# Kernel tuning notes

Measured on AMD Instinct MI355X. Metric: run time of the kernel, lower is better.

The kernel has to match this reference:

```python
import jax, jax.numpy as jnp
import numpy as np

NUM_NODES = 50000
NUM_HYPEREDGES = 10000
NUM_INCIDENCES = 800000
CHANNELS = 256
NEG_SLOPE = 0.01  # torch leaky_relu default negative_slope


def setup_inputs() -> dict:
    key = jax.random.key(0)
    k_n, k_e, k_emb, k_cw, k_lw, k_lb = jax.random.split(key, 6)
    node_idx = jax.random.randint(k_n, (NUM_INCIDENCES,), 0, NUM_NODES, dtype=jnp.int32)
    edge_idx = jax.random.randint(k_e, (NUM_INCIDENCES,), 0, NUM_HYPEREDGES, dtype=jnp.int32)
    edge_index = jnp.stack([node_idx, edge_idx], axis=0)  # [2, nnz] incidence list
    s = 1.0 / np.sqrt(CHANNELS).astype(np.float32)
    emb = jax.random.normal(k_emb, (NUM_NODES, CHANNELS), jnp.float32)  # Node2Vec embedding table
    conv_w = jax.random.normal(k_cw, (CHANNELS, CHANNELS), jnp.float32) * s  # HypergraphConv.lin (no bias)
    conv_b = jnp.zeros((CHANNELS,), jnp.float32)  # HypergraphConv.bias
    lin_w = jax.random.normal(k_lw, (CHANNELS, CHANNELS), jnp.float32) * s
    lin_b = jax.random.normal(k_lb, (CHANNELS,), jnp.float32) * s
    return {"emb": emb, "conv_w": conv_w, "conv_b": conv_b,
            "lin_w": lin_w, "lin_b": lin_b, "edge_index": edge_index}


def reference(emb, conv_w, conv_b, lin_w, lin_b, edge_index):
    node_idx, edge_idx = edge_index[0], edge_index[1]
    # HypergraphConv (use_attention=False): X' = D^-1 H B^-1 H^T (X W^T) + b
    x = emb @ conv_w.T  # [N, C]
    ones = jnp.ones((NUM_INCIDENCES,), x.dtype)
    D = jax.ops.segment_sum(ones, node_idx, num_segments=NUM_NODES)       # node degree
    Dinv = jnp.where(D > 0, 1.0 / D, 0.0)
    B = jax.ops.segment_sum(ones, edge_idx, num_segments=NUM_HYPEREDGES)  # hyperedge degree
    Binv = jnp.where(B > 0, 1.0 / B, 0.0)
    # node -> hyperedge aggregation
    e = jax.ops.segment_sum(x[node_idx], edge_idx, num_segments=NUM_HYPEREDGES) * Binv[:, None]  # [E, C]
    # hyperedge -> node aggregation
    n = jax.ops.segment_sum(e[edge_idx], node_idx, num_segments=NUM_NODES) * Dinv[:, None] + conv_b  # [N, C]
    y = jax.nn.leaky_relu(n, NEG_SLOPE)
    g = y.T @ y  # [C, C] Gram
    out = jax.nn.leaky_relu(g @ lin_w.T + lin_b, NEG_SLOPE)
    return out
```

## Files before the change

### kernel.cpp

```cpp
#include <hip/hip_runtime.h>

#define N_NODES 50000
#define N_EDGES 10000
#define NNZ     800000
#define C       256
#define SLOPE   0.01f
#define KTOT    50176
#define KCHUNK  512
#define NZB     98
#define MPAD    10048

#define NB      250
#define EB_E    40
#define EB_N    200
#define CHUNK   3125
#define CAP     6000

#define EAGG_G  157
#define NAGG_G  784

#define OFF_CC_E    0
#define OFF_CC_N    1024
#define OFF_CUR_E   2048
#define OFF_CUR_N   3072
#define ZERO_BYTES  4096
#define OFF_CB_E    266240
#define OFF_CB_N    267264
#define OFF_RS_N    268288
#define OFF_RS_E    468480
#define OFF_BUF_E   508672
#define OFF_BUF_N   3708672
#define OFF_CSR_E   6908672
#define OFF_CSR_N   10108672
#define OFF_EMBH    13308672
#define OFF_YT      13308672
#define OFF_EACC    39000064
#define OFF_E2      44144640
#define OFF_CWH     49289216
#define OFF_PART    49420288

typedef __attribute__((ext_vector_type(8))) short short8;
typedef __attribute__((ext_vector_type(4))) float floatx4;

static __device__ __forceinline__ unsigned short f2bf(float f) {
    unsigned int u = __float_as_uint(f);
    u = (u + 0x7fffu + ((u >> 16) & 1u)) >> 16;
    return (unsigned short)u;
}

static __device__ __forceinline__ void acc_bf8(const uint4 d, float* a) {
    a[0] += __uint_as_float(d.x << 16);
    a[1] += __uint_as_float(d.x & 0xffff0000u);
    a[2] += __uint_as_float(d.y << 16);
    a[3] += __uint_as_float(d.y & 0xffff0000u);
    a[4] += __uint_as_float(d.z << 16);
    a[5] += __uint_as_float(d.z & 0xffff0000u);
    a[6] += __uint_as_float(d.w << 16);
    a[7] += __uint_as_float(d.w & 0xffff0000u);
}

__global__ __launch_bounds__(256) void zero_kernel(float4* __restrict__ p, int n4) {
    int i = blockIdx.x * 256 + threadIdx.x;
    if (i < n4) p[i] = make_float4(0.f, 0.f, 0.f, 0.f);
}

#define PREP_EMB_BLOCKS 6251
#define PREP_CW_BLOCKS  32
__global__ __launch_bounds__(256) void prep_kernel(const float4* __restrict__ emb4,
                                                   uint4* __restrict__ embh4,
                                                   const float4* __restrict__ cw4,
                                                   uint4* __restrict__ cwh4,
                                                   const int* __restrict__ node_idx,
                                                   const int* __restrict__ edge_idx,
                                                   int* __restrict__ cc_e,
                                                   int* __restrict__ cc_n) {
    __shared__ int he[NB], hn[NB];
    int b = blockIdx.x, tid = threadIdx.x;
    if (b < PREP_EMB_BLOCKS) {
        int i = b * 256 + tid;
        if (i >= 1600032) return;
        uint4 o = {0u, 0u, 0u, 0u};
        if (i < 1600000) {
            float4 f0 = emb4[2 * i], f1 = emb4[2 * i + 1];
            o.x = f2bf(f0.x) | ((unsigned)f2bf(f0.y) << 16);
            o.y = f2bf(f0.z) | ((unsigned)f2bf(f0.w) << 16);
            o.z = f2bf(f1.x) | ((unsigned)f2bf(f1.y) << 16);
            o.w = f2bf(f1.z) | ((unsigned)f2bf(f1.w) << 16);
        }
        int node = i >> 5, c = i & 31;
        embh4[(size_t)(((c >> 2) * 50001 + node) << 2) + (c & 3)] = o;
    } else if (b < PREP_EMB_BLOCKS + PREP_CW_BLOCKS) {
        int i = (b - PREP_EMB_BLOCKS) * 256 + tid;
        float4 f0 = cw4[2 * i], f1 = cw4[2 * i + 1];
        uint4 o;
        o.x = f2bf(f0.x) | ((unsigned)f2bf(f0.y) << 16);
        o.y = f2bf(f0.z) | ((unsigned)f2bf(f0.w) << 16);
        o.z = f2bf(f1.x) | ((unsigned)f2bf(f1.y) << 16);
        o.w = f2bf(f1.z) | ((unsigned)f2bf(f1.w) << 16);
        cwh4[i] = o;
    } else {
        int base = (b - PREP_EMB_BLOCKS - PREP_CW_BLOCKS) * CHUNK;
        for (int i = tid; i < NB; i += 256) { he[i] = 0; hn[i] = 0; }
        __syncthreads();
        for (int i = tid; i < CHUNK; i += 256) {
            atomicAdd(&he[edge_idx[base + i] / EB_E], 1);
            atomicAdd(&hn[node_idx[base + i] / EB_N], 1);
        }
        __syncthreads();
        for (int k = tid; k < NB; k += 256) {
            if (he[k]) atomicAdd(&cc_e[k], he[k]);
            if (hn[k]) atomicAdd(&cc_n[k], hn[k]);
        }
    }
}

__global__ __launch_bounds__(256) void coarse_scan_kernel(const int* __restrict__ cc_e,
                                                          const int* __restrict__ cc_n,
                                                          int* __restrict__ cb_e,
                                                          int* __restrict__ cb_n) {
    __shared__ int tmp[256];
    int tid = threadIdx.x;
    int v = (tid < NB) ? cc_e[tid] : 0;
    tmp[tid] = v;
    __syncthreads();
    for (int off = 1; off < 256; off <<= 1) {
        int t = (tid >= off) ? tmp[tid - off] : 0;
        __syncthreads();
        tmp[tid] += t;
        __syncthreads();
    }
    if (tid < NB) cb_e[tid + 1] = tmp[tid];
    if (tid == 0) cb_e[0] = 0;
    __syncthreads();
    v = (tid < NB) ? cc_n[tid] : 0;
    tmp[tid] = v;
    __syncthreads();
    for (int off = 1; off < 256; off <<= 1) {
        int t = (tid >= off) ? tmp[tid - off] : 0;
        __syncthreads();
        tmp[tid] += t;
        __syncthreads();
    }
    if (tid < NB) cb_n[tid + 1] = tmp[tid];
    if (tid == 0) cb_n[0] = 0;
}

__global__ __launch_bounds__(256) void bucket_scatter_kernel(const int* __restrict__ node_idx,
                                                             const int* __restrict__ edge_idx,
                                                             const int* __restrict__ cb_e,
                                                             const int* __restrict__ cb_n,
                                                             int* __restrict__ cur_e,
                                                             int* __restrict__ cur_n,
                                                             int* __restrict__ buf_e,
                                                             int* __restrict__ buf_n) {
    __shared__ int he[NB], hn[NB], be[NB], bn[NB];
    int tid = threadIdx.x;
    int base = blockIdx.x * CHUNK;
    for (int i = tid; i < NB; i += 256) { he[i] = 0; hn[i] = 0; }
    __syncthreads();
    int pe[13], pn[13];
    #pragma unroll
    for (int k = 0; k < 13; k++) {
        int i = tid + k * 256;
        if (i < CHUNK) {
            int e = edge_idx[base + i], v = node_idx[base + i];
            int ke = e / EB_E, kn = v / EB_N;
            pe[k] = (ke << 12) | atomicAdd(&he[ke], 1);
            pn[k] = (kn << 12) | atomicAdd(&hn[kn], 1);
        }
    }
    __syncthreads();
    for (int k = tid; k < NB; k += 256) {
        int c = he[k];
        be[k] = cb_e[k] + (c ? atomicAdd(&cur_e[k], c) : 0);
        int cn = hn[k];
        bn[k] = cb_n[k] + (cn ? atomicAdd(&cur_n[k], cn) : 0);
    }
    __syncthreads();
    #pragma unroll
    for (int k = 0; k < 13; k++) {
        int i = tid + k * 256;
        if (i < CHUNK) {
            int e = edge_idx[base + i], v = node_idx[base + i];
            int ke = pe[k] >> 12, oe = pe[k] & 4095;
            buf_e[be[ke] + oe] = (v << 6) | (e - ke * EB_E);
            int kn = pn[k] >> 12, on = pn[k] & 4095;
            buf_n[bn[kn] + on] = (e << 8) | (v - kn * EB_N);
        }
    }
}

__global__ __launch_bounds__(256) void bucket_sort_kernel(const int* __restrict__ buf_e,
                                                          const int* __restrict__ buf_n,
                                                          const int* __restrict__ cb_e,
                                                          const int* __restrict__ cb_n,
                                                          unsigned short* __restrict__ csr_e,
                                                          unsigned short* __restrict__ csr_n,
                                                          int* __restrict__ rs_e,
                                                          int* __restrict__ rs_n) {
    __shared__ int A[CAP];
    __shared__ int h[EB_N], bs[EB_N];
    int tid = threadIdx.x;
    bool edgeSide = blockIdx.x < NB;
    int k = edgeSide ? blockIdx.x : blockIdx.x - NB;
    int eb = edgeSide ? EB_E : EB_N;
    int shift = edgeSide ? 6 : 8;
    int mask = (1 << shift) - 1;
    const int* cb  = edgeSide ? cb_e : cb_n;
    const int* buf = edgeSide ? buf_e : buf_n;
    unsigned short* csr = edgeSide ? csr_e : csr_n;
    int* rs        = edgeSide ? rs_e : rs_n;
    int base = cb[k];
    int cnt = cb[k + 1] - base;
    for (int i = tid; i < eb; i += 256) h[i] = 0;
    __syncthreads();
    for (int i = tid; i < cnt; i += 256) {
        int it = buf[base + i];
        if (i < CAP) A[i] = it;
        atomicAdd(&h[it & mask], 1);
    }
    __syncthreads();
    if (tid == 0) {
        int s = 0;
        for (int j = 0; j < eb; j++) { bs[j] = s; s += h[j]; }
    }
    __syncthreads();
    for (int j = tid; j < eb; j += 256) {
        rs[k * eb + j] = base + bs[j];
        h[j] = 0;
    }
    if (tid == 0 && k == NB - 1) rs[edgeSide ? N_EDGES : N_NODES] = NNZ;
    __syncthreads();
    for (int i = tid; i < cnt; i += 256) {
        int it = (i < CAP) ? A[i] : buf[base + i];
        int loc = it & mask;
        int off = bs[loc] + atomicAdd(&h[loc], 1);
        csr[base + off] = (unsigned short)(it >> shift);
    }
}

__global__ __launch_bounds__(256) void edge_aggregate_kernel(const uint4* __restrict__ embh4,
                                                             const unsigned short* __restrict__ csr_e,
                                                             const int* __restrict__ rs_e,
                                                             unsigned short* __restrict__ e_acc_h) {
    int sid = blockIdx.x & 7, g = blockIdx.x >> 3;
    const uint4* __restrict__ tbl = embh4 + (size_t)sid * 50001 * 4;
    int tid = threadIdx.x;
    int w = tid >> 6, lane = tid & 63;
    int qw = lane >> 2, c4 = lane & 3;
    int e = g * 64 + w * 16 + qw;
    int s = 0, t = 0;
    if (e < N_EDGES) { s = rs_e[e]; t = rs_e[e + 1]; }
    float a[8] = {0.f, 0.f, 0.f, 0.f, 0.f, 0.f, 0.f, 0.f};
    for (int i = s; i < t; i += 4) {
        int n0 = csr_e[i];
        int n1 = (i + 1 < t) ? (int)csr_e[i + 1] : N_NODES;
        int n2 = (i + 2 < t) ? (int)csr_e[i + 2] : N_NODES;
        int n3 = (i + 3 < t) ? (int)csr_e[i + 3] : N_NODES;
        uint4 d0 = tbl[n0 * 4 + c4];
        uint4 d1 = tbl[n1 * 4 + c4];
        uint4 d2 = tbl[n2 * 4 + c4];
        uint4 d3 = tbl[n3 * 4 + c4];
        acc_bf8(d0, a); acc_bf8(d1, a); acc_bf8(d2, a); acc_bf8(d3, a);
    }
    uint4 o;
    o.x = f2bf(a[0]) | ((unsigned)f2bf(a[1]) << 16);
    o.y = f2bf(a[2]) | ((unsigned)f2bf(a[3]) << 16);
    o.z = f2bf(a[4]) | ((unsigned)f2bf(a[5]) << 16);
    o.w = f2bf(a[6]) | ((unsigned)f2bf(a[7]) << 16);
    ((uint4*)(e_acc_h + (size_t)e * C + sid * 32))[c4] = o;
}

__global__ __launch_bounds__(256) void edge_gemm_mfma_kernel(const unsigned short* __restrict__ e_acc_h,
                                                             const unsigned short* __restrict__ cwh,
                                                             const int* __restrict__ rs_e,
                                                             unsigned short* __restrict__ e2h) {
    __shared__ __align__(16) unsigned short As[64 * 72];
    __shared__ __align__(16) unsigned short Bs[64 * 72];
    int i0 = blockIdx.x * 64, j0 = blockIdx.y * 64;
    int tid = threadIdx.x;
    int w = tid >> 6, lane = tid & 63;
    int col = lane & 15, quad = lane >> 4;
    floatx4 acc[4] = {};
    for (int step = 0; step < 4; step++) {
        int kb = step * 64;
        __syncthreads();
        #pragma unroll
        for (int l = 0; l < 2; l++) {
            int slot = tid + l * 256;
            int row = slot >> 3, grp = slot & 7;
            uint4 da = *(const uint4*)(e_acc_h + (size_t)(i0 + row) * C + kb + grp * 8);
            *(uint4*)(&As[row * 72 + grp * 8]) = da;
            uint4 db = *(const uint4*)(cwh + (size_t)(j0 + row) * C + kb + grp * 8);
            *(uint4*)(&Bs[row * 72 + grp * 8]) = db;
        }
        __syncthreads();
        #pragma unroll
        for (int sub = 0; sub < 2; sub++) {
            short8 a = *(const short8*)(&As[(w * 16 + col) * 72 + sub * 32 + quad * 8]);
            #pragma unroll
            for (int jt = 0; jt < 4; jt++) {
                short8 b = *(const short8*)(&Bs[(jt * 16 + col) * 72 + sub * 32 + quad * 8]);
                acc[jt] = __builtin_amdgcn_mfma_f32_16x16x32_bf16(a, b, acc[jt], 0, 0, 0);
            }
        }
    }
    #pragma unroll
    for (int r = 0; r < 4; r++) {
        int m = i0 + w * 16 + quad * 4 + r;
        int deg = (m < N_EDGES) ? rs_e[m + 1] - rs_e[m] : 0;
        float binv = (deg > 0) ? 1.0f / (float)deg : 0.0f;
        #pragma unroll
        for (int jt = 0; jt < 4; jt++) {
            int ch = j0 + jt * 16 + col;
            e2h[(size_t)((ch >> 5) * MPAD + m) * 32 + (ch & 31)] = f2bf(acc[jt][r] * binv);
        }
    }
}

__global__ __launch_bounds__(256) void node_aggregate_t_kernel(const uint4* __restrict__ e2h4,
                                                               const unsigned short* __restrict__ csr_n,
                                                               const int* __restrict__ rs_n,
                                                               const float* __restrict__ conv_b,
                                                               unsigned short* __restrict__ yT) {
    __shared__ unsigned short T[32][66];
    int sid = blockIdx.x & 7, g = blockIdx.x >> 3;
    const uint4* __restrict__ tbl = e2h4 + (size_t)sid * MPAD * 4;
    int tid = threadIdx.x;
    int w = tid >> 6, lane = tid & 63;
    int q = lane >> 2, c4 = lane & 3;
    int n = g * 64 + w * 16 + q;
    int s = 0, t = 0;
    if (n < N_NODES) { s = rs_n[n]; t = rs_n[n + 1]; }
    float4 b0 = ((const float4*)conv_b)[sid * 8 + c4 * 2];
    float4 b1 = ((const float4*)conv_b)[sid * 8 + c4 * 2 + 1];
    float a[8] = {0.f, 0.f, 0.f, 0.f, 0.f, 0.f, 0.f, 0.f};
    for (int i = s; i < t; i += 4) {
        int r0 = csr_n[i];
        int r1 = (i + 1 < t) ? (int)csr_n[i + 1] : N_EDGES;
        int r2 = (i + 2 < t) ? (int)csr_n[i + 2] : N_EDGES;
        int r3 = (i + 3 < t) ? (int)csr_n[i + 3] : N_EDGES;
        uint4 d0 = tbl[r0 * 4 + c4];
        uint4 d1 = tbl[r1 * 4 + c4];
        uint4 d2 = tbl[r2 * 4 + c4];
        uint4 d3 = tbl[r3 * 4 + c4];
        acc_bf8(d0, a); acc_bf8(d1, a); acc_bf8(d2, a); acc_bf8(d3, a);
    }
    float dinv = (t > s) ? 1.0f / (float)(t - s) : 0.0f;
    float bb[8] = {b0.x, b0.y, b0.z, b0.w, b1.x, b1.y, b1.z, b1.w};
    #pragma unroll
    for (int jj = 0; jj < 8; jj++) {
        float r = a[jj] * dinv + bb[jj];
        r = (r > 0.f) ? r : SLOPE * r;
        if (n >= N_NODES) r = 0.f;
        T[c4 * 8 + jj][w * 16 + q] = f2bf(r);
    }
    __syncthreads();
    int rr = tid >> 3, cc = tid & 7;
    uint4 o;
    o.x = T[rr][cc * 8 + 0] | ((unsigned)T[rr][cc * 8 + 1] << 16);
    o.y = T[rr][cc * 8 + 2] | ((unsigned)T[rr][cc * 8 + 3] << 16);
    o.z = T[rr][cc * 8 + 4] | ((unsigned)T[rr][cc * 8 + 5] << 16);
    o.w = T[rr][cc * 8 + 6] | ((unsigned)T[rr][cc * 8 + 7] << 16);
    *(uint4*)(yT + (size_t)(sid * 32 + rr) * KTOT + g * 64 + cc * 8) = o;
}

__global__ __launch_bounds__(256) void gram_mfma_kernel(const unsigned short* __restrict__ yT,
                                                        float* __restrict__ part) {
    static const int PI[10] = {0, 0, 0, 0, 1, 1, 1, 2, 2, 3};
    static const int PJ[10] = {0, 1, 2, 3, 1, 2, 3, 2, 3, 3};
    __shared__ __align__(16) unsigned short As[64 * 72];
    __shared__ __align__(16) unsigned short Bs[64 * 72];
    int i0 = PI[blockIdx.x] * 64, j0 = PJ[blockIdx.x] * 64;
    bool diag = (i0 == j0);
    int kb0 = blockIdx.y * KCHUNK;
    int tid = threadIdx.x;
    int w = tid >> 6, lane = tid & 63;
    int col = lane & 15, quad = lane >> 4;
    floatx4 acc[4] = {};
    for (int step = 0; step < KCHUNK / 64; step++) {
        int kb = kb0 + step * 64;
        __syncthreads();
        #pragma unroll
        for (int l = 0; l < 2; l++) {
            int slot = tid + l * 256;
            int row = slot >> 3, grp = slot & 7;
            uint4 da = *(const uint4*)(yT + (size_t)(i0 + row) * KTOT + kb + grp * 8);
            *(uint4*)(&As[row * 72 + grp * 8]) = da;
            if (!diag) {
                uint4 db = *(const uint4*)(yT + (size_t)(j0 + row) * KTOT + kb + grp * 8);
                *(uint4*)(&Bs[row * 72 + grp * 8]) = db;
            }
        }
        __syncthreads();
        const unsigned short* Bb = diag ? As : Bs;
        #pragma unroll
        for (int sub = 0; sub < 2; sub++) {
            short8 a = *(const short8*)(&As[(w * 16 + col) * 72 + sub * 32 + quad * 8]);
            #pragma unroll
            for (int jt = 0; jt < 4; jt++) {
                short8 b = *(const short8*)(&Bb[(jt * 16 + col) * 72 + sub * 32 + quad * 8]);
                acc[jt] = __builtin_amdgcn_mfma_f32_16x16x32_bf16(a, b, acc[jt], 0, 0, 0);
            }
        }
    }
    float* slab = part + ((size_t)blockIdx.y * 10 + blockIdx.x) * 4096;
    #pragma unroll
    for (int jt = 0; jt < 4; jt++)
        #pragma unroll
        for (int r = 0; r < 4; r++)
            slab[(w * 16 + quad * 4 + r) * 64 + jt * 16 + col] = acc[jt][r];
}

__global__ __launch_bounds__(256) void greduce_out_kernel(const float* __restrict__ part,
                                                          const float* __restrict__ lin_w,
                                                          const float* __restrict__ lin_b,
                                                          float* __restrict__ out) {
    __shared__ float gs[C];
    int i = blockIdx.x, j = threadIdx.x;
    int a = i >> 6, b = j >> 6;
    int lo = min(a, b), hi = max(a, b);
    int t = lo * (7 - lo) / 2 + hi;
    int li = (a <= b) ? (i & 63) : (j & 63);
    int lj = (a <= b) ? (j & 63) : (i & 63);
    const float* p = part + (size_t)t * 4096 + li * 64 + lj;
    float s = 0.f;
    for (int z = 0; z < NZB; z++) s += p[(size_t)z * 40960];
    gs[j] = s;
    __syncthreads();
    float acc = lin_b[j];
    const float* wrow = lin_w + (size_t)j * C;
    for (int k = 0; k < C; k++) acc += gs[k] * wrow[k];
    out[(size_t)i * C + j] = (acc > 0.f) ? acc : SLOPE * acc;
}

extern "C" void kernel_launch(void* const* d_in, const int* in_sizes, int n_in,
                              void* d_out, int out_size, void* d_ws, size_t ws_size,
                              hipStream_t stream) {
    const float* emb    = (const float*)d_in[0];
    const float* conv_w = (const float*)d_in[1];
    const float* conv_b = (const float*)d_in[2];
    const float* lin_w  = (const float*)d_in[3];
    const float* lin_b  = (const float*)d_in[4];
    const int*   eidx   = (const int*)d_in[5];
    const int* node_idx = eidx;
    const int* edge_idx = eidx + NNZ;

    char* ws = (char*)d_ws;
    int* cc_e  = (int*)(ws + OFF_CC_E);
    int* cc_n  = (int*)(ws + OFF_CC_N);
    int* cur_e = (int*)(ws + OFF_CUR_E);
    int* cur_n = (int*)(ws + OFF_CUR_N);
    int* cb_e  = (int*)(ws + OFF_CB_E);
    int* cb_n  = (int*)(ws + OFF_CB_N);
    int* rs_n  = (int*)(ws + OFF_RS_N);
    int* rs_e  = (int*)(ws + OFF_RS_E);
    int* buf_e = (int*)(ws + OFF_BUF_E);
    int* buf_n = (int*)(ws + OFF_BUF_N);
    unsigned short* csr_e = (unsigned short*)(ws + OFF_CSR_E);
    unsigned short* csr_n = (unsigned short*)(ws + OFF_CSR_N);
    uint4* embh4 = (uint4*)(ws + OFF_EMBH);
    unsigned short* e_acc_h = (unsigned short*)(ws + OFF_EACC);
    unsigned short* e2h = (unsigned short*)(ws + OFF_E2);
    unsigned short* cwh = (unsigned short*)(ws + OFF_CWH);
    unsigned short* yT  = (unsigned short*)(ws + OFF_YT);
    float* part = (float*)(ws + OFF_PART);
    float* out = (float*)d_out;

    zero_kernel<<<1, 256, 0, stream>>>((float4*)ws, ZERO_BYTES / 16);

    prep_kernel<<<PREP_EMB_BLOCKS + PREP_CW_BLOCKS + 256, 256, 0, stream>>>(
        (const float4*)emb, embh4, (const float4*)conv_w, (uint4*)cwh,
        node_idx, edge_idx, cc_e, cc_n);

    coarse_scan_kernel<<<1, 256, 0, stream>>>(cc_e, cc_n, cb_e, cb_n);

    bucket_scatter_kernel<<<256, 256, 0, stream>>>(node_idx, edge_idx, cb_e, cb_n,
                                                   cur_e, cur_n, buf_e, buf_n);

    bucket_sort_kernel<<<2 * NB, 256, 0, stream>>>(buf_e, buf_n, cb_e, cb_n,
                                                   csr_e, csr_n, rs_e, rs_n);

    edge_aggregate_kernel<<<8 * EAGG_G, 256, 0, stream>>>(embh4, csr_e, rs_e, e_acc_h);

    edge_gemm_mfma_kernel<<<dim3(MPAD / 64, C / 64), 256, 0, stream>>>(e_acc_h, cwh, rs_e, e2h);

    node_aggregate_t_kernel<<<8 * NAGG_G, 256, 0, stream>>>((const uint4*)e2h, csr_n, rs_n,
                                                            conv_b, yT);

    gram_mfma_kernel<<<dim3(10, NZB), 256, 0, stream>>>(yT, part);

    greduce_out_kernel<<<C, 256, 0, stream>>>(part, lin_w, lin_b, out);
}
```

Measured before the change: 302.3 us.

## Split each hyperedge across four lanes and add nontemporal loads/stores

Result: slower. 328.4 us (+8.6%).

```diff
diff --git a/kernel.cpp b/kernel.cpp
--- a/kernel.cpp
+++ b/kernel.cpp
@@ -16,7 +16,7 @@
 #define CHUNK   3125
 #define CAP     6000
 
-#define EAGG_G  157
+#define EAGG_G  628
 #define NAGG_G  784
 
 #define OFF_CC_E    0
@@ -41,11 +41,21 @@
 
 typedef __attribute__((ext_vector_type(8))) short short8;
 typedef __attribute__((ext_vector_type(4))) float floatx4;
+typedef __attribute__((ext_vector_type(4))) unsigned int uintx4;
 
 static __device__ __forceinline__ unsigned short f2bf(float f) {
     unsigned int u = __float_as_uint(f);
     u = (u + 0x7fffu + ((u >> 16) & 1u)) >> 16;
     return (unsigned short)u;
+}
+
+static __device__ __forceinline__ int ntu16(const unsigned short* p) {
+    return (int)__builtin_nontemporal_load(p);
+}
+
+static __device__ __forceinline__ void ntst16(void* p, uint4 o) {
+    uintx4 v = {o.x, o.y, o.z, o.w};
+    __builtin_nontemporal_store(v, (uintx4*)p);
 }
 
 static __device__ __forceinline__ void acc_bf8(const uint4 d, float* a) {
@@ -247,28 +257,35 @@
     const uint4* __restrict__ tbl = embh4 + (size_t)sid * 50001 * 4;
     int tid = threadIdx.x;
     int w = tid >> 6, lane = tid & 63;
-    int qw = lane >> 2, c4 = lane & 3;
-    int e = g * 64 + w * 16 + qw;
+    int grp = lane >> 4, q = (lane >> 2) & 3, c4 = lane & 3;
+    int e = g * 16 + w * 4 + grp;
     int s = 0, t = 0;
     if (e < N_EDGES) { s = rs_e[e]; t = rs_e[e + 1]; }
     float a[8] = {0.f, 0.f, 0.f, 0.f, 0.f, 0.f, 0.f, 0.f};
-    for (int i = s; i < t; i += 4) {
-        int n0 = csr_e[i];
-        int n1 = (i + 1 < t) ? (int)csr_e[i + 1] : N_NODES;
-        int n2 = (i + 2 < t) ? (int)csr_e[i + 2] : N_NODES;
-        int n3 = (i + 3 < t) ? (int)csr_e[i + 3] : N_NODES;
+    for (int i = s + q; i < t; i += 16) {
+        int n0 = ntu16(csr_e + i);
+        int n1 = (i + 4  < t) ? ntu16(csr_e + i + 4)  : N_NODES;
+        int n2 = (i + 8  < t) ? ntu16(csr_e + i + 8)  : N_NODES;
+        int n3 = (i + 12 < t) ? ntu16(csr_e + i + 12) : N_NODES;
         uint4 d0 = tbl[n0 * 4 + c4];
         uint4 d1 = tbl[n1 * 4 + c4];
         uint4 d2 = tbl[n2 * 4 + c4];
         uint4 d3 = tbl[n3 * 4 + c4];
         acc_bf8(d0, a); acc_bf8(d1, a); acc_bf8(d2, a); acc_bf8(d3, a);
     }
-    uint4 o;
-    o.x = f2bf(a[0]) | ((unsigned)f2bf(a[1]) << 16);
-    o.y = f2bf(a[2]) | ((unsigned)f2bf(a[3]) << 16);
-    o.z = f2bf(a[4]) | ((unsigned)f2bf(a[5]) << 16);
-    o.w = f2bf(a[6]) | ((unsigned)f2bf(a[7]) << 16);
-    ((uint4*)(e_acc_h + (size_t)e * C + sid * 32))[c4] = o;
+    #pragma unroll
+    for (int off = 4; off <= 8; off <<= 1) {
+        #pragma unroll
+        for (int jj = 0; jj < 8; jj++) a[jj] += __shfl_xor(a[jj], off);
+    }
+    if (q == 0) {
+        uint4 o;
+        o.x = f2bf(a[0]) | ((unsigned)f2bf(a[1]) << 16);
+        o.y = f2bf(a[2]) | ((unsigned)f2bf(a[3]) << 16);
+        o.z = f2bf(a[4]) | ((unsigned)f2bf(a[5]) << 16);
+        o.w = f2bf(a[6]) | ((unsigned)f2bf(a[7]) << 16);
+        ntst16(e_acc_h + (size_t)e * C + sid * 32 + c4 * 8, o);
+    }
 }
 
 __global__ __launch_bounds__(256) void edge_gemm_mfma_kernel(const unsigned short* __restrict__ e_acc_h,
@@ -336,10 +353,10 @@
     float4 b1 = ((const float4*)conv_b)[sid * 8 + c4 * 2 + 1];
     float a[8] = {0.f, 0.f, 0.f, 0.f, 0.f, 0.f, 0.f, 0.f};
     for (int i = s; i < t; i += 4) {
-        int r0 = csr_n[i];
-        int r1 = (i + 1 < t) ? (int)csr_n[i + 1] : N_EDGES;
-        int r2 = (i + 2 < t) ? (int)csr_n[i + 2] : N_EDGES;
-        int r3 = (i + 3 < t) ? (int)csr_n[i + 3] : N_EDGES;
+        int r0 = ntu16(csr_n + i);
+        int r1 = (i + 1 < t) ? ntu16(csr_n + i + 1) : N_EDGES;
+        int r2 = (i + 2 < t) ? ntu16(csr_n + i + 2) : N_EDGES;
+        int r3 = (i + 3 < t) ? ntu16(csr_n + i + 3) : N_EDGES;
         uint4 d0 = tbl[r0 * 4 + c4];
         uint4 d1 = tbl[r1 * 4 + c4];
         uint4 d2 = tbl[r2 * 4 + c4];
@@ -362,7 +379,7 @@
     o.y = T[rr][cc * 8 + 2] | ((unsigned)T[rr][cc * 8 + 3] << 16);
     o.z = T[rr][cc * 8 + 4] | ((unsigned)T[rr][cc * 8 + 5] << 16);
     o.w = T[rr][cc * 8 + 6] | ((unsigned)T[rr][cc * 8 + 7] << 16);
-    *(uint4*)(yT + (size_t)(sid * 32 + rr) * KTOT + g * 64 + cc * 8) = o;
+    ntst16(yT + (size_t)(sid * 32 + rr) * KTOT + g * 64 + cc * 8, o);
 }
 
 __global__ __launch_bounds__(256) void gram_mfma_kernel(const unsigned short* __restrict__ yT,
```
